# Kernel tuning notes

Measured on AMD Instinct MI355X. Metric: run time of the kernel, lower is better.

Reference implementation:

```python
import jax, jax.numpy as jnp
import numpy as np
from jax import lax

# data_spacing = (dx, dy, dz) matched to spatial axes (1, 2, 3) of (B, S, R, C)
SPACING = (2.0, 1.5, 1.5)


def _pad_edge(X, axis):
    pad = [(0, 0)] * X.ndim
    pad[axis] = (1, 1)
    return jnp.pad(X, pad, mode='edge')  # torch ReplicationPad equivalent


def _dc(X, axis, d):
    # central difference with replication padding: (X[i+1]-X[i-1])/(2d)
    Xp = _pad_edge(X, axis)
    n = X.shape[axis]
    return (lax.slice_in_dim(Xp, 2, n + 2, axis=axis)
            - lax.slice_in_dim(Xp, 0, n, axis=axis)) / (2.0 * d)


def _df(X, axis, d):
    # forward difference: (X[i+1]-X[i])/d
    Xp = _pad_edge(X, axis)
    n = X.shape[axis]
    return (lax.slice_in_dim(Xp, 2, n + 2, axis=axis)
            - lax.slice_in_dim(Xp, 1, n + 1, axis=axis)) / d


def _db(X, axis, d):
    # backward difference: (X[i]-X[i-1])/d
    Xp = _pad_edge(X, axis)
    n = X.shape[axis]
    return (lax.slice_in_dim(Xp, 1, n + 1, axis=axis)
            - lax.slice_in_dim(Xp, 0, n, axis=axis)) / d


def _set_bc_neumann(X):
    # crop 1-voxel boundary, then replicate-pad it back (Neumann / zero-flux BC)
    inner = X[:, 1:-1, 1:-1, 1:-1]
    return jnp.pad(inner, ((0, 0), (1, 1), (1, 1), (1, 1)), mode='edge')


def setup_inputs() -> dict:
    key = jax.random.key(0)
    k1, k2, k3 = jax.random.split(key, 3)
    B, S, R, C = 8, 128, 192, 192
    t = jax.random.normal(k1, (B,), dtype=jnp.float32)
    batch_P = jax.random.normal(k2, (B, S, R, C), dtype=jnp.float32)
    D = jax.random.uniform(k3, (B, S, R, C), dtype=jnp.float32)  # scalar diffusivity field
    return {"t": t, "batch_P": batch_P, "D": D}


def reference(t, batch_P, D):
    P = _set_bc_neumann(batch_P)
    dx, dy, dz = SPACING
    # F = |grad P|^2 via central differences
    F = (_dc(P, 1, dx) ** 2 + _dc(P, 2, dy) ** 2 + _dc(P, 3, dz) ** 2)
    # G = laplacian P via backward(forward) differences per axis
    G = (_db(_df(P, 1, dx), 1, dx)
         + _db(_df(P, 2, dy), 2, dy)
         + _db(_df(P, 3, dz), 3, dz))
    # dP/dt = -1/2 |grad P|^2 - D * laplacian P
    return -0.5 * F - D * G
```

## Files before the change

kernel.cpp:

```cpp
#include <hip/hip_runtime.h>


#define BB 8
#define SS 128
#define RR 192
#define CC 192

typedef float v4f __attribute__((ext_vector_type(4)));

__device__ __forceinline__ float stencil_pt(float pc, float pSm, float pSp,
                                            float pRm, float pRp,
                                            float pCm, float pCp, float d)
{
    const float inv2dx = 0.25f;
    const float inv2dy = 1.0f / 3.0f;
    const float inv2dz = 1.0f / 3.0f;
    const float invdx2 = 0.25f;
    const float invdy2 = 1.0f / 2.25f;
    const float invdz2 = 1.0f / 2.25f;

    float dcx = (pSp - pSm) * inv2dx;
    float dcy = (pRp - pRm) * inv2dy;
    float dcz = (pCp - pCm) * inv2dz;
    float F = dcx * dcx + dcy * dcy + dcz * dcz;
    float G = (pSp - 2.0f * pc + pSm) * invdx2
            + (pRp - 2.0f * pc + pRm) * invdy2
            + (pCp - 2.0f * pc + pCm) * invdz2;
    return -0.5f * F - d * G;
}

__global__ __launch_bounds__(192) void flowp_kernel(
    const float* __restrict__ P,
    const float* __restrict__ D,
    float* __restrict__ out)
{
    const int tx = threadIdx.x;
    const int k0 = tx << 2;
    const int j  = blockIdx.y * 4 + threadIdx.y;
    const int bz = blockIdx.z;
    const int i  = bz & (SS - 1);
    const int b  = bz >> 7;

    const int ci  = min(max(i,     1), SS - 2);
    const int cim = min(max(i - 1, 1), SS - 2);
    const int cip = min(max(i + 1, 1), SS - 2);
    const int cj  = min(max(j,     1), RR - 2);
    const int cjm = min(max(j - 1, 1), RR - 2);
    const int cjp = min(max(j + 1, 1), RR - 2);

    const int bS = b * SS;
    const int rowC  = ((bS + ci ) * RR + cj ) * CC;
    const int rowSm = ((bS + cim) * RR + cj ) * CC;
    const int rowSp = ((bS + cip) * RR + cj ) * CC;
    const int rowRm = ((bS + ci ) * RR + cjm) * CC;
    const int rowRp = ((bS + ci ) * RR + cjp) * CC;

    const bool e0 = (tx == 0);
    const bool e1 = (tx == 47);

    const v4f c4 = *(const v4f*)(P + rowC + k0);
    const int cmI = e0 ? 1      : k0 - 1;
    const int cpI = e1 ? CC - 2 : k0 + 4;
    const float cm = P[rowC + cmI];
    const float cp = P[rowC + cpI];
    const float w1 = e0 ? c4.y : c4.x;
    const float w2 = c4.y;
    const float w3 = c4.z;
    const float w4 = e1 ? c4.z : c4.w;

    v4f nSm = *(const v4f*)(P + rowSm + k0);
    v4f nSp = *(const v4f*)(P + rowSp + k0);
    v4f nRm = *(const v4f*)(P + rowRm + k0);
    v4f nRp = *(const v4f*)(P + rowRp + k0);
    nSm.x = e0 ? nSm.y : nSm.x;  nSm.w = e1 ? nSm.z : nSm.w;
    nSp.x = e0 ? nSp.y : nSp.x;  nSp.w = e1 ? nSp.z : nSp.w;
    nRm.x = e0 ? nRm.y : nRm.x;  nRm.w = e1 ? nRm.z : nRm.w;
    nRp.x = e0 ? nRp.y : nRp.x;  nRp.w = e1 ? nRp.z : nRp.w;

    const int idxO = ((bS + i) * RR + j) * CC + k0;
    const v4f d4 = __builtin_nontemporal_load((const v4f*)(D + idxO));

    v4f o;
    o.x = stencil_pt(w1, nSm.x, nSp.x, nRm.x, nRp.x, cm, w2, d4.x);
    o.y = stencil_pt(w2, nSm.y, nSp.y, nRm.y, nRp.y, w1, w3, d4.y);
    o.z = stencil_pt(w3, nSm.z, nSp.z, nRm.z, nRp.z, w2, w4, d4.z);
    o.w = stencil_pt(w4, nSm.w, nSp.w, nRm.w, nRp.w, w3, cp, d4.w);

    __builtin_nontemporal_store(o, (v4f*)(out + idxO));
}

extern "C" void kernel_launch(void* const* d_in, const int* in_sizes, int n_in,
                              void* d_out, int out_size, void* d_ws, size_t ws_size,
                              hipStream_t stream) {
    const float* P = (const float*)d_in[1];
    const float* D = (const float*)d_in[2];
    float* out = (float*)d_out;

    dim3 block(48, 4, 1);
    dim3 grid(1, RR / 4, BB * SS);
    flowp_kernel<<<grid, block, 0, stream>>>(P, D, out);
}
```

Baseline: 344.8 us.

## March along S axis per workgroup with register reuse and prefetch

Each workgroup now processes a chunk of 16 consecutive S-planes instead of a single plane. The S-neighbour rows are kept in registers and rotated, and the next plane's rows and D values are prefetched one iteration ahead. The grid is flattened and swizzled across chunk and batch indices, and launch bounds now request 6 blocks per CU. The goal is to cut redundant global loads of P and to hide memory latency, at the cost of fewer workgroups, more registers per thread and less parallelism.

```diff
diff --git a/kernel.cpp b/kernel.cpp
--- a/kernel.cpp
+++ b/kernel.cpp
@@ -5,8 +5,37 @@
 #define SS 128
 #define RR 192
 #define CC 192
+#define PLANE (RR * CC)
+#define SC 16
+#define NCHUNK (SS / SC)
+#define NWG (48 * BB * NCHUNK)
 
 typedef float v4f __attribute__((ext_vector_type(4)));
+
+struct Row6 { float cm, w1, w2, w3, w4, cp; };
+
+__device__ __forceinline__ v4f load_row4(const float* __restrict__ row, int k0,
+                                         bool e0, bool e1)
+{
+    v4f c4 = *(const v4f*)(row + k0);
+    c4.x = e0 ? c4.y : c4.x;
+    c4.w = e1 ? c4.z : c4.w;
+    return c4;
+}
+
+__device__ __forceinline__ Row6 load_row6(const float* __restrict__ row, int k0,
+                                          int kcm, int kcp, bool e0, bool e1)
+{
+    Row6 r;
+    v4f c4 = *(const v4f*)(row + k0);
+    r.cm = row[kcm];
+    r.cp = row[kcp];
+    r.w1 = e0 ? c4.y : c4.x;
+    r.w2 = c4.y;
+    r.w3 = c4.z;
+    r.w4 = e1 ? c4.z : c4.w;
+    return r;
+}
 
 __device__ __forceinline__ float stencil_pt(float pc, float pSm, float pSp,
                                             float pRm, float pRp,
@@ -29,64 +58,74 @@
     return -0.5f * F - d * G;
 }
 
-__global__ __launch_bounds__(192) void flowp_kernel(
+__global__ __launch_bounds__(192, 6) void flowp_kernel(
     const float* __restrict__ P,
     const float* __restrict__ D,
     float* __restrict__ out)
 {
     const int tx = threadIdx.x;
     const int k0 = tx << 2;
-    const int j  = blockIdx.y * 4 + threadIdx.y;
-    const int bz = blockIdx.z;
-    const int i  = bz & (SS - 1);
-    const int b  = bz >> 7;
+    const bool e0 = (tx == 0);
+    const bool e1 = (tx == 47);
+    const int kcm = e0 ? 1 : k0 - 1;
+    const int kcp = e1 ? CC - 2 : k0 + 4;
 
-    const int ci  = min(max(i,     1), SS - 2);
-    const int cim = min(max(i - 1, 1), SS - 2);
-    const int cip = min(max(i + 1, 1), SS - 2);
+    const int wg    = blockIdx.x;
+    const int swz   = (wg & 7) * (NWG / 8) + (wg >> 3);
+    const int jg    = swz % 48;
+    const int bc    = swz / 48;
+    const int b     = bc & 7;
+    const int chunk = bc >> 3;
+    const int i0    = chunk * SC;
+
+    const int j   = jg * 4 + threadIdx.y;
     const int cj  = min(max(j,     1), RR - 2);
     const int cjm = min(max(j - 1, 1), RR - 2);
     const int cjp = min(max(j + 1, 1), RR - 2);
 
-    const int bS = b * SS;
-    const int rowC  = ((bS + ci ) * RR + cj ) * CC;
-    const int rowSm = ((bS + cim) * RR + cj ) * CC;
-    const int rowSp = ((bS + cip) * RR + cj ) * CC;
-    const int rowRm = ((bS + ci ) * RR + cjm) * CC;
-    const int rowRp = ((bS + ci ) * RR + cjp) * CC;
+    const float* Pb    = P + b * (SS * PLANE);
+    const float* rowC  = Pb + cj  * CC;
+    const float* rowJm = Pb + cjm * CC;
+    const float* rowJp = Pb + cjp * CC;
 
-    const bool e0 = (tx == 0);
-    const bool e1 = (tx == 47);
+    const int pm = min(max(i0 - 1, 1), SS - 2);
+    int offC = min(max(i0, 1), SS - 2) * PLANE;
+    int offP = min(i0 + 1, SS - 2) * PLANE;
 
-    const v4f c4 = *(const v4f*)(P + rowC + k0);
-    const int cmI = e0 ? 1      : k0 - 1;
-    const int cpI = e1 ? CC - 2 : k0 + 4;
-    const float cm = P[rowC + cmI];
-    const float cp = P[rowC + cpI];
-    const float w1 = e0 ? c4.y : c4.x;
-    const float w2 = c4.y;
-    const float w3 = c4.z;
-    const float w4 = e1 ? c4.z : c4.w;
+    v4f  aM = load_row4(rowC + pm * PLANE, k0, e0, e1);
+    Row6 aC = load_row6(rowC + offC, k0, kcm, kcp, e0, e1);
+    Row6 aP = load_row6(rowC + offP, k0, kcm, kcp, e0, e1);
+    v4f  Rm = load_row4(rowJm + offC, k0, e0, e1);
+    v4f  Rp = load_row4(rowJp + offC, k0, e0, e1);
 
-    v4f nSm = *(const v4f*)(P + rowSm + k0);
-    v4f nSp = *(const v4f*)(P + rowSp + k0);
-    v4f nRm = *(const v4f*)(P + rowRm + k0);
-    v4f nRp = *(const v4f*)(P + rowRp + k0);
-    nSm.x = e0 ? nSm.y : nSm.x;  nSm.w = e1 ? nSm.z : nSm.w;
-    nSp.x = e0 ? nSp.y : nSp.x;  nSp.w = e1 ? nSp.z : nSp.w;
-    nRm.x = e0 ? nRm.y : nRm.x;  nRm.w = e1 ? nRm.z : nRm.w;
-    nRp.x = e0 ? nRp.y : nRp.x;  nRp.w = e1 ? nRp.z : nRp.w;
+    int idxO = ((b * SS + i0) * RR + j) * CC + k0;
+    v4f d4 = __builtin_nontemporal_load((const v4f*)(D + idxO));
 
-    const int idxO = ((bS + i) * RR + j) * CC + k0;
-    const v4f d4 = __builtin_nontemporal_load((const v4f*)(D + idxO));
+#pragma unroll
+    for (int s = 0; s < SC; ++s) {
+        const int offN = min(offP + PLANE, (SS - 2) * PLANE);
+        v4f nRm = Rm, nRp = Rp, nD = d4;
+        Row6 nC = aP;
+        if (s < SC - 1) {
+            nRm = load_row4(rowJm + offP, k0, e0, e1);
+            nRp = load_row4(rowJp + offP, k0, e0, e1);
+            nC  = load_row6(rowC + offN, k0, kcm, kcp, e0, e1);
+            nD  = __builtin_nontemporal_load((const v4f*)(D + idxO + PLANE));
+        }
 
-    v4f o;
-    o.x = stencil_pt(w1, nSm.x, nSp.x, nRm.x, nRp.x, cm, w2, d4.x);
-    o.y = stencil_pt(w2, nSm.y, nSp.y, nRm.y, nRp.y, w1, w3, d4.y);
-    o.z = stencil_pt(w3, nSm.z, nSp.z, nRm.z, nRp.z, w2, w4, d4.z);
-    o.w = stencil_pt(w4, nSm.w, nSp.w, nRm.w, nRp.w, w3, cp, d4.w);
+        v4f o;
+        o.x = stencil_pt(aC.w1, aM.x, aP.w1, Rm.x, Rp.x, aC.cm, aC.w2, d4.x);
+        o.y = stencil_pt(aC.w2, aM.y, aP.w2, Rm.y, Rp.y, aC.w1, aC.w3, d4.y);
+        o.z = stencil_pt(aC.w3, aM.z, aP.w3, Rm.z, Rp.z, aC.w2, aC.w4, d4.z);
+        o.w = stencil_pt(aC.w4, aM.w, aP.w4, Rm.w, Rp.w, aC.w3, aC.cp, d4.w);
+        __builtin_nontemporal_store(o, (v4f*)(out + idxO));
 
-    __builtin_nontemporal_store(o, (v4f*)(out + idxO));
+        aM.x = aC.w1; aM.y = aC.w2; aM.z = aC.w3; aM.w = aC.w4;
+        aC = aP; aP = nC;
+        Rm = nRm; Rp = nRp; d4 = nD;
+        offC = offP; offP = offN;
+        idxO += PLANE;
+    }
 }
 
 extern "C" void kernel_launch(void* const* d_in, const int* in_sizes, int n_in,
@@ -97,6 +136,6 @@
     float* out = (float*)d_out;
 
     dim3 block(48, 4, 1);
-    dim3 grid(1, RR / 4, BB * SS);
+    dim3 grid(NWG, 1, 1);
     flowp_kernel<<<grid, block, 0, stream>>>(P, D, out);
 }
```

Measured after the change: 361.3 us. 4.8% more time.
